# Kernel optimization log

Measured on AMD Instinct MI355X. Metric: run time of the kernel, lower is better.

The kernel has to match this reference:

```python
import jax, jax.numpy as jnp
import numpy as np
import math

# Fixed rendering constants (from module-level source)
FOV_X = 60.0
FOV_Y = 60.0
NEAR = 0.1
FAR = 10000.0
SCALE_MODIFIER = 1.0
MAX_FREQUENCY = 128.0
NUM_TOTAL_FREQUENCIES = 1024
GAUSSIAN_ONLY = False
COV_DILATION = 0.3  # low-pass dilation as in 3DGS EWA splatting

N_PRIM = 512
TOP_K = 8
IMG_H = 200
IMG_W = 200


def _quat_to_rotmat(q):
    # q: [N,4] (r, x, y, z), normalized
    q = q / (jnp.linalg.norm(q, axis=-1, keepdims=True) + 1e-8)
    r, x, y, z = q[:, 0], q[:, 1], q[:, 2], q[:, 3]
    R = jnp.stack([
        jnp.stack([1 - 2 * (y * y + z * z), 2 * (x * y - r * z), 2 * (x * z + r * y)], -1),
        jnp.stack([2 * (x * y + r * z), 1 - 2 * (x * x + z * z), 2 * (y * z - r * x)], -1),
        jnp.stack([2 * (x * z - r * y), 2 * (y * z + r * x), 1 - 2 * (x * x + y * y)], -1),
    ], axis=-2)  # [N,3,3]
    return R


def _forward(colors, opacities, background_color, positions, scales, rotations,
             topk_wave_coefficients, topk_wave_indices, cam_position,
             view_matrix, VP_matrix, image_width, image_height):
    H, W = image_height, image_width
    N = positions.shape[0]
    tan_x = math.tan(math.radians(FOV_X * 0.5))
    tan_y = math.tan(math.radians(FOV_Y * 0.5))
    fx = W / (2.0 * tan_x)
    fy = H / (2.0 * tan_y)

    # --- 3D covariance: Sigma = R diag(s^2) R^T, s = exp(log_scales) * modifier
    R = _quat_to_rotmat(rotations)                     # [N,3,3]
    s = jnp.exp(scales) * SCALE_MODIFIER               # [N,3]
    Sigma = jnp.einsum('nij,nj,nkj->nik', R, s * s, R)  # [N,3,3]

    # --- projection
    p_hom = jnp.concatenate([positions, jnp.ones((N, 1), positions.dtype)], -1)  # [N,4]
    t_cam = jnp.einsum('ij,nj->ni', view_matrix, p_hom)[:, :3]                   # [N,3] camera space
    clip = jnp.einsum('ij,nj->ni', VP_matrix, p_hom)                             # [N,4]
    wclip = clip[:, 3:4]
    ndc = clip[:, :2] / jnp.where(jnp.abs(wclip) > 1e-6, wclip, 1e-6)
    px = (ndc * 0.5 + 0.5) * jnp.array([W, H], positions.dtype)                  # [N,2] pixel center
    depth = t_cam[:, 2]

    # --- EWA 2D covariance: cov2d = J Wr Sigma Wr^T J^T + dilation
    tz = jnp.maximum(depth, NEAR)
    tx, ty = t_cam[:, 0], t_cam[:, 1]
    zeros = jnp.zeros_like(tz)
    J = jnp.stack([
        jnp.stack([fx / tz, zeros, -fx * tx / (tz * tz)], -1),
        jnp.stack([zeros, fy / tz, -fy * ty / (tz * tz)], -1),
    ], axis=-2)                                         # [N,2,3]
    Wr = view_matrix[:3, :3]
    M = jnp.einsum('nij,jk->nik', J, Wr)                # [N,2,3]
    cov2d = jnp.einsum('nab,nbc,ndc->nad', M, Sigma, M) # [N,2,2]
    A = cov2d[:, 0, 0] + COV_DILATION
    B = cov2d[:, 0, 1]
    C = cov2d[:, 1, 1] + COV_DILATION
    det = jnp.maximum(A * C - B * B, 1e-12)
    conA, conB, conC = C / det, -B / det, A / det       # conic (inverse cov)

    # --- pixel grid [H*W]
    ys = jnp.arange(H, dtype=positions.dtype) + 0.5
    xs = jnp.arange(W, dtype=positions.dtype) + 0.5
    gy, gx = jnp.meshgrid(ys, xs, indexing='ij')
    gx, gy = gx.ravel(), gy.ravel()

    dx = px[:, 0:1] - gx[None, :]                       # [N,HW]
    dy = px[:, 1:2] - gy[None, :]
    power = -0.5 * (conA[:, None] * dx * dx + conC[:, None] * dy * dy) - conB[:, None] * dx * dy
    G = jnp.exp(jnp.minimum(power, 0.0))                # [N,HW]

    # --- periodic (Gabor) modulation along projected primary axis of each primitive
    if GAUSSIAN_ONLY:
        wave = 1.0
    else:
        a3 = R[:, :, 0]                                  # local first axis, world space [N,3]
        a2 = jnp.einsum('nij,nj->ni', M, a3)             # projected to screen [N,2]
        a2 = a2 / (jnp.linalg.norm(a2, axis=-1, keepdims=True) + 1e-8)
        tcoord = (dx * a2[:, 0:1] + dy * a2[:, 1:2]) / W  # [N,HW], normalized coord
        freqs = topk_wave_indices.astype(positions.dtype) * (MAX_FREQUENCY / NUM_TOTAL_FREQUENCIES)  # [N,K]
        wave = jnp.zeros_like(tcoord)
        for k in range(topk_wave_indices.shape[1]):      # small fixed K, unrolled
            wave = wave + topk_wave_coefficients[:, k:k + 1] * jnp.cos(
                2.0 * jnp.pi * freqs[:, k:k + 1] * tcoord)

    alpha = jnp.clip(opacities * G * wave, 0.0, 0.99)   # [N,HW]
    valid = (depth > NEAR) & (wclip[:, 0] > 1e-4)
    alpha = jnp.where(valid[:, None], alpha, 0.0)

    # --- depth sort + front-to-back alpha compositing
    order = jnp.argsort(depth)
    alpha_s = alpha[order]
    colors_s = colors[order]
    Tprod = jnp.cumprod(1.0 - alpha_s, axis=0)           # inclusive transmittance
    T_excl = jnp.concatenate([jnp.ones((1, alpha_s.shape[1]), alpha_s.dtype), Tprod[:-1]], 0)
    img = jnp.einsum('nc,np->cp', colors_s, alpha_s * T_excl)  # [3,HW]
    img = img + background_color[:, None] * Tprod[-1][None, :]
    return img.reshape(3, H, W)


def setup_inputs() -> dict:
    key = jax.random.key(0)
    ks = jax.random.split(key, 10)
    N, K = N_PRIM, TOP_K
    colors = jax.random.uniform(ks[0], (N, 3), jnp.float32)
    opacities = 0.8 * jax.random.uniform(ks[1], (N, 1), jnp.float32)
    background_color = jnp.zeros((3,), jnp.float32)
    # positions inside the view frustum: z in [4,12], xy in [-3,3]
    xy = jax.random.uniform(ks[2], (N, 2), jnp.float32, -3.0, 3.0)
    z = jax.random.uniform(ks[3], (N, 1), jnp.float32, 4.0, 12.0)
    positions = jnp.concatenate([xy, z], -1)
    scales = -2.5 + 0.3 * jax.random.normal(ks[4], (N, 3), jnp.float32)  # log-scales
    rotations = jax.random.normal(ks[5], (N, 4), jnp.float32)
    topk_wave_coefficients = 0.1 * jax.random.normal(ks[6], (N, K), jnp.float32)
    topk_wave_indices = jax.random.randint(ks[7], (N, K), 1, NUM_TOTAL_FREQUENCIES).astype(jnp.int32)
    cam_position = jnp.zeros((3,), jnp.float32)
    view_matrix = jnp.eye(4, dtype=jnp.float32)
    tan_x = math.tan(math.radians(FOV_X * 0.5))
    tan_y = math.tan(math.radians(FOV_Y * 0.5))
    P = jnp.array([[1.0 / tan_x, 0, 0, 0],
                   [0, 1.0 / tan_y, 0, 0],
                   [0, 0, FAR / (FAR - NEAR), -FAR * NEAR / (FAR - NEAR)],
                   [0, 0, 1.0, 0]], jnp.float32)
    VP_matrix = P @ view_matrix
    return {
        'colors': colors, 'opacities': opacities, 'background_color': background_color,
        'positions': positions, 'scales': scales, 'rotations': rotations,
        'topk_wave_coefficients': topk_wave_coefficients, 'topk_wave_indices': topk_wave_indices,
        'cam_position': cam_position, 'view_matrix': view_matrix, 'VP_matrix': VP_matrix,
        'image_width': IMG_W, 'image_height': IMG_H,
    }


def reference(colors, opacities, background_color, positions, scales, rotations,
              topk_wave_coefficients, topk_wave_indices, cam_position,
              view_matrix, VP_matrix, image_width, image_height):
    return _forward(colors, opacities, background_color, positions, scales, rotations,
                    topk_wave_coefficients, topk_wave_indices, cam_position,
                    view_matrix, VP_matrix, image_width, image_height)
```

## Files before the change

kernel.cpp:

```cpp
#include <hip/hip_runtime.h>
#include <math.h>

#define NPRIM   512
#define TOPK    8
#define PSTRIDE 28
#define IMG     200
#define NPIX    (IMG * IMG)
#define NSEG    8
#define SEGSZ   (NPRIM / NSEG)
#define TILE    64
#define TILES_X (IMG / 8)
#define NTILES  (TILES_X * TILES_X)
#define GRID    209


__global__ __launch_bounds__(NPRIM) void fused_kernel(
    const float* __restrict__ colors,
    const float* __restrict__ opacities,
    const float* __restrict__ positions,
    const float* __restrict__ scales,
    const float* __restrict__ rotations,
    const float* __restrict__ wcoef,
    const int*   __restrict__ widx,
    const float* __restrict__ view,
    const float* __restrict__ VP,
    const float* __restrict__ bg,
    float* __restrict__ out)
{
    __shared__ float  lds[NPRIM * PSTRIDE];
    __shared__ float4 sbb[NPRIM];
    __shared__ union {
        unsigned long long sk[2][NPRIM];
        float4 part[NSEG * TILE];
    } u;

    const int n = threadIdx.x;

    {
        float4 q   = ((const float4*)rotations)[n];
        float4 cfa = ((const float4*)wcoef)[2*n];
        float4 cfb = ((const float4*)wcoef)[2*n+1];
        int4   ia  = ((const int4*)widx)[2*n];
        int4   ib  = ((const int4*)widx)[2*n+1];
        float sc0 = scales[n*3+0], sc1 = scales[n*3+1], sc2 = scales[n*3+2];
        float px_ = positions[n*3+0], py_ = positions[n*3+1], pz_ = positions[n*3+2];
        float col0 = colors[n*3+0], col1 = colors[n*3+1], col2 = colors[n*3+2];
        float opa = opacities[n];

        const float tanx = 0.57735026918962576451f;
        const float fx = IMG / (2.0f * tanx);
        const float fy = IMG / (2.0f * tanx);

        float qr = q.x, qx = q.y, qy = q.z, qz = q.w;
        float qn = sqrtf(qr*qr + qx*qx + qy*qy + qz*qz) + 1e-8f;
        qr /= qn; qx /= qn; qy /= qn; qz /= qn;
        float R00 = 1.f - 2.f*(qy*qy + qz*qz), R01 = 2.f*(qx*qy - qr*qz), R02 = 2.f*(qx*qz + qr*qy);
        float R10 = 2.f*(qx*qy + qr*qz), R11 = 1.f - 2.f*(qx*qx + qz*qz), R12 = 2.f*(qy*qz - qr*qx);
        float R20 = 2.f*(qx*qz - qr*qy), R21 = 2.f*(qy*qz + qr*qx), R22 = 1.f - 2.f*(qx*qx + qy*qy);

        float s0 = expf(sc0); s0 *= s0;
        float s1 = expf(sc1); s1 *= s1;
        float s2 = expf(sc2); s2 *= s2;

        float S00 = R00*R00*s0 + R01*R01*s1 + R02*R02*s2;
        float S01 = R00*R10*s0 + R01*R11*s1 + R02*R12*s2;
        float S02 = R00*R20*s0 + R01*R21*s1 + R02*R22*s2;
        float S11 = R10*R10*s0 + R11*R11*s1 + R12*R12*s2;
        float S12 = R10*R20*s0 + R11*R21*s1 + R12*R22*s2;
        float S22 = R20*R20*s0 + R21*R21*s1 + R22*R22*s2;

        float t0 = view[0]*px_ + view[1]*py_ + view[2]*pz_  + view[3];
        float t1 = view[4]*px_ + view[5]*py_ + view[6]*pz_  + view[7];
        float t2 = view[8]*px_ + view[9]*py_ + view[10]*pz_ + view[11];
        float c0 = VP[0]*px_  + VP[1]*py_  + VP[2]*pz_  + VP[3];
        float c1 = VP[4]*px_  + VP[5]*py_  + VP[6]*pz_  + VP[7];
        float w  = VP[12]*px_ + VP[13]*py_ + VP[14]*pz_ + VP[15];

        float denom = (fabsf(w) > 1e-6f) ? w : 1e-6f;
        float pxs = (c0/denom * 0.5f + 0.5f) * (float)IMG;
        float pys = (c1/denom * 0.5f + 0.5f) * (float)IMG;

        float depth = t2;
        float tz = fmaxf(depth, 0.1f);
        float invz = 1.f / tz;
        float J00 = fx*invz, J02 = -fx*t0*invz*invz;
        float J11 = fy*invz, J12 = -fy*t1*invz*invz;

        float M00 = J00*view[0] + J02*view[8];
        float M01 = J00*view[1] + J02*view[9];
        float M02 = J00*view[2] + J02*view[10];
        float M10 = J11*view[4] + J12*view[8];
        float M11 = J11*view[5] + J12*view[9];
        float M12 = J11*view[6] + J12*view[10];

        float T00 = M00*S00 + M01*S01 + M02*S02;
        float T01 = M00*S01 + M01*S11 + M02*S12;
        float T02 = M00*S02 + M01*S12 + M02*S22;
        float T10 = M10*S00 + M11*S01 + M12*S02;
        float T11 = M10*S01 + M11*S11 + M12*S12;
        float T12 = M10*S02 + M11*S12 + M12*S22;
        float cA = T00*M00 + T01*M01 + T02*M02 + 0.3f;
        float cB = T00*M10 + T01*M11 + T02*M12;
        float cC = T10*M10 + T11*M11 + T12*M12 + 0.3f;
        float det  = fmaxf(cA*cC - cB*cB, 1e-12f);
        float idet = 1.f / det;
        float conA = cC*idet, conB = -cB*idet, conC = cA*idet;

        float a2x = M00*R00 + M01*R10 + M02*R20;
        float a2y = M10*R00 + M11*R10 + M12*R20;
        float an = sqrtf(a2x*a2x + a2y*a2y) + 1e-8f;
        a2x = (a2x/an) * (1.0f/(float)IMG);
        a2y = (a2y/an) * (1.0f/(float)IMG);

        bool valid = (depth > 0.1f) && (w > 1e-4f);
        float op = valid ? opa : 0.0f;

        float rx = valid ? sqrtf(fmaxf(30.f * cA, 0.f)) : -1e30f;
        float ry = valid ? sqrtf(fmaxf(30.f * cC, 0.f)) : -1e30f;

        unsigned db = __float_as_uint(depth);
        db = (db & 0x80000000u) ? ~db : (db | 0x80000000u);
        unsigned long long kreg = ((unsigned long long)db << 32) | (unsigned)n;

        int ls = 0;
#pragma unroll
        for (int k = 2; k <= NPRIM; k <<= 1) {
#pragma unroll
            for (int j = k >> 1; j > 0; j >>= 1) {
                unsigned long long vp;
                if (j >= 64) {
                    u.sk[ls][n] = kreg;
                    __syncthreads();
                    vp = u.sk[ls][n ^ j];
                    ls ^= 1;
                } else {
                    vp = __shfl_xor(kreg, j, 64);
                }
                bool takeMin = (((n & k) == 0) == ((n & j) == 0));
                unsigned long long mn = (kreg < vp) ? kreg : vp;
                unsigned long long mx = (kreg < vp) ? vp : kreg;
                kreg = takeMin ? mn : mx;
            }
        }
        int* sinv = (int*)u.sk[0];
        sinv[(unsigned)kreg] = n;
        __syncthreads();
        int rank = sinv[n];

        const float om = 0.78539816339744830962f;
        float4* e4 = (float4*)(lds + rank * PSTRIDE);
        e4[0] = make_float4(pxs, pys, conA, conB);
        e4[1] = make_float4(conC, a2x, a2y, op);
        e4[2] = make_float4(col0, col1, col2, 0.f);
        e4[3] = cfa;
        e4[4] = cfb;
        e4[5] = make_float4(om*(float)ia.x, om*(float)ia.y, om*(float)ia.z, om*(float)ia.w);
        e4[6] = make_float4(om*(float)ib.x, om*(float)ib.y, om*(float)ib.z, om*(float)ib.w);
        sbb[rank] = make_float4(pxs, pys, rx, ry);
    }
    __syncthreads();

    const int lane = n & 63;
    const int wv   = n >> 6;
    const float4 bb = sbb[wv * SEGSZ + lane];
    const float* seg = lds + (wv * SEGSZ) * PSTRIDE;
    const float bg0 = bg[0], bg1 = bg[1], bg2 = bg[2];

    for (int t = blockIdx.x; t < NTILES; t += GRID) {
        const int tx = t % TILES_X, ty = t / TILES_X;
        const int x  = tx*8 + (lane & 7);
        const int y  = ty*8 + (lane >> 3);
        const float gx = (float)x + 0.5f, gy = (float)y + 0.5f;

        const float tcx = (float)(tx*8) + 4.0f, tcy = (float)(ty*8) + 4.0f;
        bool active = (fabsf(bb.x - tcx) <= bb.z + 3.5f) &&
                      (fabsf(bb.y - tcy) <= bb.w + 3.5f);
        unsigned long long mask = __ballot(active);

        float T = 1.f, cr = 0.f, cg = 0.f, cb = 0.f;
        while (mask) {
            int j = __ffsll((unsigned long long)mask) - 1;
            mask &= mask - 1;
            const float* h = seg + j * PSTRIDE;
            float4 q0 = *(const float4*)(h);
            float4 q1 = *(const float4*)(h + 4);
            float dx = q0.x - gx, dy = q0.y - gy;
            float pw = -0.5f*(q0.z*dx*dx + q1.x*dy*dy) - q0.w*dx*dy;
            if (__any(pw > -15.0f)) {
                float4 q2 = *(const float4*)(h + 8);
                float4 c0 = *(const float4*)(h + 12), c1 = *(const float4*)(h + 16);
                float4 w0 = *(const float4*)(h + 20), w1 = *(const float4*)(h + 24);
                float G = __expf(fminf(pw, 0.f));
                float tt = dx*q1.y + dy*q1.z;
                float wave = c0.x*__cosf(w0.x*tt) + c0.y*__cosf(w0.y*tt)
                           + c0.z*__cosf(w0.z*tt) + c0.w*__cosf(w0.w*tt)
                           + c1.x*__cosf(w1.x*tt) + c1.y*__cosf(w1.y*tt)
                           + c1.z*__cosf(w1.z*tt) + c1.w*__cosf(w1.w*tt);
                float a = fminf(fmaxf(q1.w * G * wave, 0.f), 0.99f);
                float wgt = a * T;
                cr += q2.x*wgt; cg += q2.y*wgt; cb += q2.z*wgt;
                T *= (1.f - a);
            }
        }
        u.part[wv*TILE + lane] = make_float4(cr, cg, cb, T);

        __syncthreads();

        if (n < TILE) {
            float Ta = 1.f, fr = 0.f, fg = 0.f, fb = 0.f;
#pragma unroll
            for (int s = 0; s < NSEG; ++s) {
                float4 v = u.part[s*TILE + lane];
                fr += Ta * v.x; fg += Ta * v.y; fb += Ta * v.z;
                Ta *= v.w;
            }
            const int p = y*IMG + x;
            out[p]          = fr + bg0*Ta;
            out[NPIX + p]   = fg + bg1*Ta;
            out[2*NPIX + p] = fb + bg2*Ta;
        }
        __syncthreads();
    }
}

extern "C" void kernel_launch(void* const* d_in, const int* in_sizes, int n_in,
                              void* d_out, int out_size, void* d_ws, size_t ws_size,
                              hipStream_t stream) {
    const float* colors  = (const float*)d_in[0];
    const float* opac    = (const float*)d_in[1];
    const float* bg      = (const float*)d_in[2];
    const float* pos     = (const float*)d_in[3];
    const float* scales  = (const float*)d_in[4];
    const float* rot     = (const float*)d_in[5];
    const float* wcoef   = (const float*)d_in[6];
    const int*   widx    = (const int*)d_in[7];
    const float* view    = (const float*)d_in[9];
    const float* VP      = (const float*)d_in[10];
    (void)d_ws; (void)ws_size;

    hipLaunchKernelGGL(fused_kernel, dim3(GRID), dim3(NPRIM), 0, stream,
                       colors, opac, pos, scales, rot, wcoef, widx, view, VP,
                       bg, (float*)d_out);
}
```

Before: 88.89 us.

## Write primitives unsorted with permutation index and batch per-tile merges to one barrier

Primitive records are now written to LDS at their original index before the sort, and a perm array maps sorted position to primitive. This removes the inverse-permutation scatter and its barrier. The tile loop is unrolled to a fixed three tiles per block, with all partial results staged in LDS and merged by three waves after a single barrier, instead of two barriers per tile. The cost is one extra indirect LDS read per primitive visit and a larger union for partials. The union now sizes to the 3x8x64 float4 partial array.

```diff
diff --git a/kernel.cpp b/kernel.cpp
--- a/kernel.cpp
+++ b/kernel.cpp
@@ -8,10 +8,10 @@
 #define NPIX    (IMG * IMG)
 #define NSEG    8
 #define SEGSZ   (NPRIM / NSEG)
-#define TILE    64
 #define TILES_X (IMG / 8)
 #define NTILES  (TILES_X * TILES_X)
 #define GRID    209
+#define TPB     3
 
 
 __global__ __launch_bounds__(NPRIM) void fused_kernel(
@@ -29,9 +29,10 @@
 {
     __shared__ float  lds[NPRIM * PSTRIDE];
     __shared__ float4 sbb[NPRIM];
+    __shared__ int    perm[NPRIM];
     __shared__ union {
         unsigned long long sk[2][NPRIM];
-        float4 part[NSEG * TILE];
+        float4 part[TPB][NSEG][SEGSZ];
     } u;
 
     const int n = threadIdx.x;
@@ -117,6 +118,17 @@
 
         float rx = valid ? sqrtf(fmaxf(30.f * cA, 0.f)) : -1e30f;
         float ry = valid ? sqrtf(fmaxf(30.f * cC, 0.f)) : -1e30f;
+
+        const float om = 0.78539816339744830962f;
+        float4* e4 = (float4*)(lds + n * PSTRIDE);
+        e4[0] = make_float4(pxs, pys, conA, conB);
+        e4[1] = make_float4(conC, a2x, a2y, op);
+        e4[2] = make_float4(col0, col1, col2, 0.f);
+        e4[3] = cfa;
+        e4[4] = cfb;
+        e4[5] = make_float4(om*(float)ia.x, om*(float)ia.y, om*(float)ia.z, om*(float)ia.w);
+        e4[6] = make_float4(om*(float)ib.x, om*(float)ib.y, om*(float)ib.z, om*(float)ib.w);
+        sbb[n] = make_float4(pxs, pys, rx, ry);
 
         unsigned db = __float_as_uint(depth);
         db = (db & 0x80000000u) ? ~db : (db | 0x80000000u);
@@ -142,31 +154,21 @@
                 kreg = takeMin ? mn : mx;
             }
         }
-        int* sinv = (int*)u.sk[0];
-        sinv[(unsigned)kreg] = n;
-        __syncthreads();
-        int rank = sinv[n];
-
-        const float om = 0.78539816339744830962f;
-        float4* e4 = (float4*)(lds + rank * PSTRIDE);
-        e4[0] = make_float4(pxs, pys, conA, conB);
-        e4[1] = make_float4(conC, a2x, a2y, op);
-        e4[2] = make_float4(col0, col1, col2, 0.f);
-        e4[3] = cfa;
-        e4[4] = cfb;
-        e4[5] = make_float4(om*(float)ia.x, om*(float)ia.y, om*(float)ia.z, om*(float)ia.w);
-        e4[6] = make_float4(om*(float)ib.x, om*(float)ib.y, om*(float)ib.z, om*(float)ib.w);
-        sbb[rank] = make_float4(pxs, pys, rx, ry);
+        perm[n] = (int)(unsigned)kreg;
     }
     __syncthreads();
 
     const int lane = n & 63;
     const int wv   = n >> 6;
-    const float4 bb = sbb[wv * SEGSZ + lane];
-    const float* seg = lds + (wv * SEGSZ) * PSTRIDE;
+    const int   pidx = perm[wv * SEGSZ + lane];
+    const float4 bb  = sbb[pidx];
+    const int*  segp = perm + wv * SEGSZ;
     const float bg0 = bg[0], bg1 = bg[1], bg2 = bg[2];
 
-    for (int t = blockIdx.x; t < NTILES; t += GRID) {
+#pragma unroll
+    for (int t3 = 0; t3 < TPB; ++t3) {
+        const int t = blockIdx.x + t3 * GRID;
+        if (t >= NTILES) break;
         const int tx = t % TILES_X, ty = t / TILES_X;
         const int x  = tx*8 + (lane & 7);
         const int y  = ty*8 + (lane >> 3);
@@ -181,7 +183,7 @@
         while (mask) {
             int j = __ffsll((unsigned long long)mask) - 1;
             mask &= mask - 1;
-            const float* h = seg + j * PSTRIDE;
+            const float* h = lds + segp[j] * PSTRIDE;
             float4 q0 = *(const float4*)(h);
             float4 q1 = *(const float4*)(h + 4);
             float dx = q0.x - gx, dy = q0.y - gy;
@@ -202,15 +204,21 @@
                 T *= (1.f - a);
             }
         }
-        u.part[wv*TILE + lane] = make_float4(cr, cg, cb, T);
-
-        __syncthreads();
-
-        if (n < TILE) {
+        u.part[t3][wv][lane] = make_float4(cr, cg, cb, T);
+    }
+
+    __syncthreads();
+
+    if (wv < TPB) {
+        const int t = blockIdx.x + wv * GRID;
+        if (t < NTILES) {
+            const int tx = t % TILES_X, ty = t / TILES_X;
+            const int x  = tx*8 + (lane & 7);
+            const int y  = ty*8 + (lane >> 3);
             float Ta = 1.f, fr = 0.f, fg = 0.f, fb = 0.f;
 #pragma unroll
             for (int s = 0; s < NSEG; ++s) {
-                float4 v = u.part[s*TILE + lane];
+                float4 v = u.part[wv][s][lane];
                 fr += Ta * v.x; fg += Ta * v.y; fb += Ta * v.z;
                 Ta *= v.w;
             }
@@ -219,7 +227,6 @@
             out[NPIX + p]   = fg + bg1*Ta;
             out[2*NPIX + p] = fb + bg2*Ta;
         }
-        __syncthreads();
     }
 }
 
```

Measured after the change: 88.36 us. About the same (-0.6%).
